# Performance work log

Measured on AMD Instinct MI355X. Metric: run time of the kernel, lower is better.

## Reference

```python
import jax, jax.numpy as jnp
import numpy as np

N = 524288   # total samples
D = 128      # embedding dim
S = 128      # samples per group (equal-size contiguous groups)
G = N // S   # number of groups = 4096
MARGIN = 2.0
K_MARGIN = 0.02
EPS = 1e-6


def setup_inputs() -> dict:
    key = jax.random.key(0)
    k1, k2, k3, k4 = jax.random.split(key, 4)
    z_r = jax.random.normal(k1, (N, D), jnp.float32)
    z_v = jax.random.normal(k2, (N, D), jnp.float32)
    labels = jax.random.randint(k3, (N,), 0, 2, dtype=jnp.int32)
    # contiguous equal-size groups: group id = index // S
    groups = (jnp.arange(N, dtype=jnp.int32) // S).astype(jnp.int32)
    var_lens = jax.random.randint(k4, (N,), 0, 100, dtype=jnp.int32)
    return {"z_r": z_r, "z_v": z_v, "labels": labels, "groups": groups, "var_lens": var_lens}


def _std1(x):
    # torch.Tensor.std default is unbiased (ddof=1)
    return jnp.std(x, axis=1, ddof=1)


def reference(z_r, z_v, labels, groups, var_lens):
    # cosine distance per row: [N]
    d = 1.0 - jnp.sum(z_r * z_v, axis=-1)

    # ----- contrastive distance-difference loss -----
    mb = labels == 0
    mp = labels == 1
    nb = mb.sum()
    npos = mp.sum()
    mean_b = jnp.sum(jnp.where(mb, d, 0.0)) / jnp.maximum(nb, 1)
    mean_p = jnp.sum(jnp.where(mp, d, 0.0)) / jnp.maximum(npos, 1)
    l_cdd = jnp.where((nb > 0) & (npos > 0),
                      jax.nn.relu(MARGIN + mean_b - mean_p), 0.0)

    # ----- per-group losses, vectorized over groups as [G, S] -----
    # groups is arange(N)//S -> contiguous equal-size groups, so reshape is exact
    vlen = var_lens.reshape(G, S).astype(jnp.float32)
    dist = d.reshape(G, S)

    vs = _std1(vlen)   # [G]
    ds = _std1(dist)   # [G]
    vz = (vlen - vlen.mean(axis=1, keepdims=True)) / (vs[:, None] + EPS)
    dz = (dist - dist.mean(axis=1, keepdims=True)) / (ds[:, None] + EPS)
    corr_loss = jnp.where((vs > 0) & (ds > 0),
                          jnp.mean((vz - dz) ** 2, axis=1), 0.0)  # [G]

    order = jnp.argsort(vlen, axis=1)
    v_sorted = jnp.take_along_axis(vlen, order, axis=1)  # [G,S]
    d_sorted = jnp.take_along_axis(dist, order, axis=1)  # [G,S]

    neigh_viol = jnp.mean(
        jax.nn.relu(d_sorted[:, :-1] - d_sorted[:, 1:] + K_MARGIN), axis=1)  # [G]

    # pairwise diffs: dv[g,i,j] = v[g,j] - v[g,i] (torch unsqueeze(0)-unsqueeze(1))
    dv = v_sorted[:, None, :] - v_sorted[:, :, None]  # [G,S,S]
    dd = d_sorted[:, None, :] - d_sorted[:, :, None]  # [G,S,S]
    mask = dv > 0
    cnt = mask.sum(axis=(1, 2))  # [G]
    viol_sum = jnp.sum(jnp.where(mask, jax.nn.relu(K_MARGIN - dd), 0.0), axis=(1, 2))
    rank_loss = jnp.where(cnt > 0, viol_sum / jnp.maximum(cnt, 1), 0.0)  # [G]

    group_losses = corr_loss + neigh_viol + rank_loss  # [G]
    sizes = jnp.full((G,), float(S), jnp.float32)
    weights = sizes / sizes.sum()
    l_pcc = jnp.sum(weights * group_losses)

    return (l_cdd, l_pcc, d)
```

## Files before the change

### kernel.cpp

```cpp
#include <hip/hip_runtime.h>
#include <hip/hip_bf16.h>

#define D_DIM   128
#define S_GRP   128
#define MARGINF 2.0f
#define KMARG   0.02f
#define EPSF    1e-6f

__global__ __launch_bounds__(256) void compute_d_kernel(
    const float* __restrict__ zr, const float* __restrict__ zv,
    const int* __restrict__ labels, float* __restrict__ out,
    double* __restrict__ wsd, int* __restrict__ wsi, int n)
{
    const int tid    = blockIdx.x * blockDim.x + threadIdx.x;
    const int wave   = tid >> 6;
    const int lane   = threadIdx.x & 63;
    const int nwaves = (gridDim.x * blockDim.x) >> 6;
    const int half   = lane >> 5;
    const int sub    = lane & 31;
    const int npairs = n >> 1;

    float accB = 0.f, accP = 0.f;
    int   cntB = 0,   cntP = 0;

    for (int pi = wave; pi < npairs; pi += nwaves) {
        const int r = 2 * pi + half;
        const float4* a = (const float4*)(zr + (size_t)r * D_DIM);
        const float4* b = (const float4*)(zv + (size_t)r * D_DIM);
        float4 x = a[sub];
        float4 y = b[sub];
        float p = x.x * y.x + x.y * y.y + x.z * y.z + x.w * y.w;
        #pragma unroll
        for (int off = 16; off; off >>= 1) p += __shfl_xor(p, off);
        if (sub == 0) {
            float dv = 1.0f - p;
            out[2 + r] = dv;
            if (labels[r] == 0) { accB += dv; cntB++; }
            else                { accP += dv; cntP++; }
        }
    }
    accB += __shfl_xor(accB, 32);
    accP += __shfl_xor(accP, 32);
    cntB += __shfl_xor(cntB, 32);
    cntP += __shfl_xor(cntP, 32);

    __shared__ float sB[4], sP[4];
    __shared__ int   iB[4], iP[4];
    const int w = threadIdx.x >> 6;
    if (lane == 0) { sB[w] = accB; sP[w] = accP; iB[w] = cntB; iP[w] = cntP; }
    __syncthreads();
    if (threadIdx.x == 0) {
        float tb = 0.f, tp = 0.f; int cb = 0, cp = 0;
        #pragma unroll
        for (int i = 0; i < 4; ++i) { tb += sB[i]; tp += sP[i]; cb += iB[i]; cp += iP[i]; }
        atomicAdd(&wsd[0], (double)tb);
        atomicAdd(&wsd[1], (double)tp);
        atomicAdd(&wsi[0], cb);
        atomicAdd(&wsi[1], cp);
    }
}

__device__ __forceinline__ float block_reduce_128(float x, volatile float* sh)
{
    #pragma unroll
    for (int off = 32; off; off >>= 1) x += __shfl_xor(x, off);
    __syncthreads();
    if ((threadIdx.x & 63) == 0) sh[threadIdx.x >> 6] = x;
    __syncthreads();
    return sh[0] + sh[1];
}

__global__ __launch_bounds__(128) void group_kernel(
    const int* __restrict__ var_lens, const float* __restrict__ dvals,
    double* __restrict__ pcc_sum)
{
    const int g = blockIdx.x;
    const int t = threadIdx.x;
    __shared__ float sv[S_GRP], sd[S_GRP], svs[S_GRP], sds[S_GRP];
    __shared__ float sred[2];

    const float v = (float)var_lens[(size_t)g * S_GRP + t];
    const float d = dvals[(size_t)g * S_GRP + t];
    sv[t] = v; sd[t] = d;

    const float mv = block_reduce_128(v, sred) * (1.0f / S_GRP);
    const float md = block_reduce_128(d, sred) * (1.0f / S_GRP);
    const float cv = v - mv, cd = d - md;

    const float ssv = block_reduce_128(cv * cv, sred);
    const float ssd = block_reduce_128(cd * cd, sred);
    const float vs  = sqrtf(ssv * (1.0f / (S_GRP - 1)));
    const float dsd = sqrtf(ssd * (1.0f / (S_GRP - 1)));

    const float vz = cv / (vs + EPSF);
    const float dz = cd / (dsd + EPSF);
    const float df = vz - dz;
    float corr = block_reduce_128(df * df, sred) * (1.0f / S_GRP);
    if (!(vs > 0.f && dsd > 0.f)) corr = 0.f;

    int rank = 0;
    #pragma unroll 8
    for (int j = 0; j < S_GRP; ++j) {
        const float vj = sv[j];
        rank += (vj < v) || (vj == v && j < t);
    }
    svs[rank] = v; sds[rank] = d;
    __syncthreads();

    float nv = 0.f;
    if (t < S_GRP - 1) nv = fmaxf(sds[t] - sds[t + 1] + KMARG, 0.f);
    const float neigh = block_reduce_128(nv, sred) * (1.0f / (S_GRP - 1));

    const float myv = svs[t], myd = sds[t];
    float viol = 0.f, cnt = 0.f;
    #pragma unroll 8
    for (int j = 0; j < S_GRP; ++j) {
        const float vj = svs[j];
        if (vj > myv) {
            cnt  += 1.f;
            viol += fmaxf(KMARG - (sds[j] - myd), 0.f);
        }
    }
    const float violT = block_reduce_128(viol, sred);
    const float cntT  = block_reduce_128(cnt,  sred);
    const float rloss = (cntT > 0.f) ? violT / cntT : 0.f;

    if (t == 0) atomicAdd(pcc_sum, (double)(corr + neigh + rloss));
}

__global__ void finalize_kernel(const double* __restrict__ wsd,
                                const int* __restrict__ wsi,
                                float* __restrict__ out, int nGroups)
{
    if (threadIdx.x == 0 && blockIdx.x == 0) {
        const int nb = wsi[0], np_ = wsi[1];
        const double mean_b = wsd[0] / (double)(nb  > 0 ? nb  : 1);
        const double mean_p = wsd[1] / (double)(np_ > 0 ? np_ : 1);
        float l = 0.f;
        if (nb > 0 && np_ > 0) {
            const double v = (double)MARGINF + mean_b - mean_p;
            l = (float)(v > 0.0 ? v : 0.0);
        }
        out[0] = l;
        out[1] = (float)(wsd[2] / (double)nGroups);
    }
}

extern "C" void kernel_launch(void* const* d_in, const int* in_sizes, int n_in,
                              void* d_out, int out_size, void* d_ws, size_t ws_size,
                              hipStream_t stream)
{
    const float* zr       = (const float*)d_in[0];
    const float* zv       = (const float*)d_in[1];
    const int*   labels   = (const int*)d_in[2];
    const int*   var_lens = (const int*)d_in[4];
    float* out = (float*)d_out;

    const int N = in_sizes[2];
    const int G = N / S_GRP;

    double* wsd = (double*)d_ws;
    int*    wsi = (int*)((char*)d_ws + 3 * sizeof(double));

    hipMemsetAsync(d_ws, 0, 3 * sizeof(double) + 2 * sizeof(int), stream);

    compute_d_kernel<<<2048, 256, 0, stream>>>(zr, zv, labels, out, wsd, wsi, N);
    group_kernel<<<G, 128, 0, stream>>>(var_lens, out + 2, wsd + 2);
    finalize_kernel<<<1, 64, 0, stream>>>(wsd, wsi, out, G);
}
```

Measured before the change: 657.7 us.

## Batch row loads per wave and replace global atomics with per-block partials

The distance kernel now loads eight row pairs per wave iteration before reducing, which raises memory-level parallelism, and it halves the grid to 1024 blocks. Per-block and per-group results are written to workspace arrays and summed by a multi-thread finalize kernel instead of double atomics. This also drops the memset launch. The atomic path is kept as a fallback when the workspace is too small, and the tail of npairs not divisible by eight would be skipped, though N here divides evenly.

```diff
diff --git a/kernel.cpp b/kernel.cpp
--- a/kernel.cpp
+++ b/kernel.cpp
@@ -7,10 +7,17 @@
 #define KMARG   0.02f
 #define EPSF    1e-6f
 
-__global__ __launch_bounds__(256) void compute_d_kernel(
+#define CD_BLOCKS  1024
+#define CD_THREADS 256
+#define U_PAIRS    8
+
+template <bool USE_PARTIALS>
+__global__ __launch_bounds__(CD_THREADS) void compute_d_kernel(
     const float* __restrict__ zr, const float* __restrict__ zv,
-    const int* __restrict__ labels, float* __restrict__ out,
-    double* __restrict__ wsd, int* __restrict__ wsi, int n)
+    const int* __restrict__ labels, float* __restrict__ dout,
+    float* __restrict__ partB, float* __restrict__ partP,
+    int* __restrict__ pcntB, int* __restrict__ pcntP,
+    double* __restrict__ wsd, int* __restrict__ wsi, int npairs)
 {
     const int tid    = blockIdx.x * blockDim.x + threadIdx.x;
     const int wave   = tid >> 6;
@@ -18,45 +25,71 @@
     const int nwaves = (gridDim.x * blockDim.x) >> 6;
     const int half   = lane >> 5;
     const int sub    = lane & 31;
-    const int npairs = n >> 1;
 
     float accB = 0.f, accP = 0.f;
     int   cntB = 0,   cntP = 0;
 
-    for (int pi = wave; pi < npairs; pi += nwaves) {
-        const int r = 2 * pi + half;
-        const float4* a = (const float4*)(zr + (size_t)r * D_DIM);
-        const float4* b = (const float4*)(zv + (size_t)r * D_DIM);
-        float4 x = a[sub];
-        float4 y = b[sub];
-        float p = x.x * y.x + x.y * y.y + x.z * y.z + x.w * y.w;
+    const int nchunks = npairs / U_PAIRS;
+
+    for (int c = wave; c < nchunks; c += nwaves) {
+        const int pair0 = c * U_PAIRS;
+        float4 x[U_PAIRS], y[U_PAIRS];
         #pragma unroll
-        for (int off = 16; off; off >>= 1) p += __shfl_xor(p, off);
+        for (int u = 0; u < U_PAIRS; ++u) {
+            const size_t r = (size_t)(2 * (pair0 + u) + half);
+            x[u] = ((const float4*)(zr + r * D_DIM))[sub];
+            y[u] = ((const float4*)(zv + r * D_DIM))[sub];
+        }
+        float p[U_PAIRS];
+        #pragma unroll
+        for (int u = 0; u < U_PAIRS; ++u)
+            p[u] = x[u].x * y[u].x + x[u].y * y[u].y
+                 + x[u].z * y[u].z + x[u].w * y[u].w;
+        #pragma unroll
+        for (int off = 16; off; off >>= 1) {
+            #pragma unroll
+            for (int u = 0; u < U_PAIRS; ++u) p[u] += __shfl_xor(p[u], off);
+        }
         if (sub == 0) {
-            float dv = 1.0f - p;
-            out[2 + r] = dv;
-            if (labels[r] == 0) { accB += dv; cntB++; }
-            else                { accP += dv; cntP++; }
-        }
-    }
-    accB += __shfl_xor(accB, 32);
-    accP += __shfl_xor(accP, 32);
-    cntB += __shfl_xor(cntB, 32);
-    cntP += __shfl_xor(cntP, 32);
-
+            #pragma unroll
+            for (int u = 0; u < U_PAIRS; ++u) {
+                const int r = 2 * (pair0 + u) + half;
+                const float dv = 1.0f - p[u];
+                dout[r] = dv;
+                if (labels[r] == 0) { accB += dv; cntB++; }
+                else                { accP += dv; cntP++; }
+            }
+        }
+    }
+
+    #pragma unroll
+    for (int off = 32; off; off >>= 1) {
+        accB += __shfl_xor(accB, off);
+        accP += __shfl_xor(accP, off);
+        cntB += __shfl_xor(cntB, off);
+        cntP += __shfl_xor(cntP, off);
+    }
     __shared__ float sB[4], sP[4];
     __shared__ int   iB[4], iP[4];
     const int w = threadIdx.x >> 6;
     if (lane == 0) { sB[w] = accB; sP[w] = accP; iB[w] = cntB; iP[w] = cntP; }
     __syncthreads();
     if (threadIdx.x == 0) {
-        float tb = 0.f, tp = 0.f; int cb = 0, cp = 0;
-        #pragma unroll
-        for (int i = 0; i < 4; ++i) { tb += sB[i]; tp += sP[i]; cb += iB[i]; cp += iP[i]; }
-        atomicAdd(&wsd[0], (double)tb);
-        atomicAdd(&wsd[1], (double)tp);
-        atomicAdd(&wsi[0], cb);
-        atomicAdd(&wsi[1], cp);
+        const float tB = sB[0] + sB[1] + sB[2] + sB[3];
+        const float tP = sP[0] + sP[1] + sP[2] + sP[3];
+        const int   cB = iB[0] + iB[1] + iB[2] + iB[3];
+        const int   cP = iP[0] + iP[1] + iP[2] + iP[3];
+        if (USE_PARTIALS) {
+            partB[blockIdx.x] = tB;
+            partP[blockIdx.x] = tP;
+            pcntB[blockIdx.x] = cB;
+            pcntP[blockIdx.x] = cP;
+        } else {
+            atomicAdd(&wsd[0], (double)tB);
+            atomicAdd(&wsd[1], (double)tP);
+            atomicAdd(&wsi[0], cB);
+            atomicAdd(&wsi[1], cP);
+        }
     }
 }
 
@@ -70,9 +103,10 @@
     return sh[0] + sh[1];
 }
 
+template <bool USE_PARTIALS>
 __global__ __launch_bounds__(128) void group_kernel(
     const int* __restrict__ var_lens, const float* __restrict__ dvals,
-    double* __restrict__ pcc_sum)
+    float* __restrict__ gl, double* __restrict__ pcc_sum)
 {
     const int g = blockIdx.x;
     const int t = threadIdx.x;
@@ -125,12 +159,64 @@
     const float cntT  = block_reduce_128(cnt,  sred);
     const float rloss = (cntT > 0.f) ? violT / cntT : 0.f;
 
-    if (t == 0) atomicAdd(pcc_sum, (double)(corr + neigh + rloss));
-}
-
-__global__ void finalize_kernel(const double* __restrict__ wsd,
-                                const int* __restrict__ wsi,
-                                float* __restrict__ out, int nGroups)
+    if (t == 0) {
+        const float total = corr + neigh + rloss;
+        if (USE_PARTIALS) gl[g] = total;
+        else              atomicAdd(pcc_sum, (double)total);
+    }
+}
+
+__global__ __launch_bounds__(256) void finalize_kernel(
+    const float* __restrict__ partB, const float* __restrict__ partP,
+    const int* __restrict__ pcntB, const int* __restrict__ pcntP,
+    const float* __restrict__ gl, float* __restrict__ out,
+    int nPart, int nGroups)
+{
+    double a0 = 0.0, a1 = 0.0, a2 = 0.0, a3 = 0.0, a4 = 0.0;
+    for (int i = threadIdx.x; i < nPart; i += 256) {
+        a0 += (double)partB[i];
+        a1 += (double)partP[i];
+        a2 += (double)pcntB[i];
+        a3 += (double)pcntP[i];
+    }
+    for (int i = threadIdx.x; i < nGroups; i += 256)
+        a4 += (double)gl[i];
+
+    #pragma unroll
+    for (int off = 32; off; off >>= 1) {
+        a0 += __shfl_xor(a0, off);
+        a1 += __shfl_xor(a1, off);
+        a2 += __shfl_xor(a2, off);
+        a3 += __shfl_xor(a3, off);
+        a4 += __shfl_xor(a4, off);
+    }
+    __shared__ double red[5][4];
+    const int w = threadIdx.x >> 6;
+    if ((threadIdx.x & 63) == 0) {
+        red[0][w] = a0; red[1][w] = a1; red[2][w] = a2; red[3][w] = a3; red[4][w] = a4;
+    }
+    __syncthreads();
+    if (threadIdx.x == 0) {
+        const double sB = red[0][0] + red[0][1] + red[0][2] + red[0][3];
+        const double sP = red[1][0] + red[1][1] + red[1][2] + red[1][3];
+        const double cB = red[2][0] + red[2][1] + red[2][2] + red[2][3];
+        const double cP = red[3][0] + red[3][1] + red[3][2] + red[3][3];
+        const double sG = red[4][0] + red[4][1] + red[4][2] + red[4][3];
+        const double mean_b = sB / (cB > 0.0 ? cB : 1.0);
+        const double mean_p = sP / (cP > 0.0 ? cP : 1.0);
+        float l = 0.f;
+        if (cB > 0.0 && cP > 0.0) {
+            const double vv = (double)MARGINF + mean_b - mean_p;
+            l = (float)(vv > 0.0 ? vv : 0.0);
+        }
+        out[0] = l;
+        out[1] = (float)(sG / (double)nGroups);
+    }
+}
+
+__global__ void finalize_atomic_kernel(const double* __restrict__ wsd,
+                                       const int* __restrict__ wsi,
+                                       float* __restrict__ out, int nGroups)
 {
     if (threadIdx.x == 0 && blockIdx.x == 0) {
         const int nb = wsi[0], np_ = wsi[1];
@@ -159,12 +245,31 @@
     const int N = in_sizes[2];
     const int G = N / S_GRP;
 
-    double* wsd = (double*)d_ws;
-    int*    wsi = (int*)((char*)d_ws + 3 * sizeof(double));
-
-    hipMemsetAsync(d_ws, 0, 3 * sizeof(double) + 2 * sizeof(int), stream);
-
-    compute_d_kernel<<<2048, 256, 0, stream>>>(zr, zv, labels, out, wsd, wsi, N);
-    group_kernel<<<G, 128, 0, stream>>>(var_lens, out + 2, wsd + 2);
-    finalize_kernel<<<1, 64, 0, stream>>>(wsd, wsi, out, G);
-}
+    const size_t need = (size_t)CD_BLOCKS * 16 + (size_t)G * 4;
+
+    if (ws_size >= need) {
+        float* partB = (float*)d_ws;
+        float* partP = partB + CD_BLOCKS;
+        int*   pcntB = (int*)(partP + CD_BLOCKS);
+        int*   pcntP = pcntB + CD_BLOCKS;
+        float* gl    = (float*)(pcntP + CD_BLOCKS);
+
+        compute_d_kernel<true><<<CD_BLOCKS, CD_THREADS, 0, stream>>>(
+            zr, zv, labels, out + 2, partB, partP, pcntB, pcntP,
+            nullptr, nullptr, N / 2);
+        group_kernel<true><<<G, 128, 0, stream>>>(var_lens, out + 2, gl, nullptr);
+        finalize_kernel<<<1, 256, 0, stream>>>(partB, partP, pcntB, pcntP, gl,
+                                               out, CD_BLOCKS, G);
+    } else {
+        double* wsd = (double*)d_ws;
+        int*    wsi = (int*)((char*)d_ws + 3 * sizeof(double));
+        hipMemsetAsync(d_ws, 0, 3 * sizeof(double) + 2 * sizeof(int), stream);
+
+        compute_d_kernel<false><<<CD_BLOCKS, CD_THREADS, 0, stream>>>(
+            zr, zv, labels, out + 2, nullptr, nullptr, nullptr, nullptr,
+            wsd, wsi, N / 2);
+        group_kernel<false><<<G, 128, 0, stream>>>(var_lens, out + 2, nullptr,
+                                                   wsd + 2);
+        finalize_atomic_kernel<<<1, 64, 0, stream>>>(wsd, wsi, out, G);
+    }
+}
```

New measurement: 555.7 us. -15.5%, faster.
